# Kernel tuning notes

Measured on AMD Instinct MI355X. Metric: run time of the kernel, lower is better.

The kernel has to match this reference:

```python
import jax, jax.numpy as jnp
import numpy as np

K = 3        # kernel_size
PAD = 1      # padding
STRIDE = 1   # stride


def conv2d(x, w, stride, pad):
    return jax.lax.conv_general_dilated(
        x, w, (stride, stride), [(pad, pad), (pad, pad)],
        dimension_numbers=('NCHW', 'OIHW', 'NCHW'))


def setup_inputs() -> dict:
    key = jax.random.key(0)
    ks = jax.random.split(key, 6)
    B, C, H, W, O = 8, 64, 64, 64, 128
    N = K * K
    x = jax.random.normal(ks[0], (B, C, H, W), jnp.float32)
    # offset (shift) conv: 2N output channels; small weights so sampled
    # positions deviate a few pixels from the regular grid
    shift_w = jax.random.normal(ks[1], (2 * N, C, 3, 3), jnp.float32) * 0.01
    shift_b = jax.random.normal(ks[2], (2 * N,), jnp.float32) * 0.5
    # modulation conv: N output channels
    mod_w = jax.random.normal(ks[3], (N, C, 3, 3), jnp.float32) * 0.01
    mod_b = jax.random.normal(ks[4], (N,), jnp.float32) * 0.1
    # final conv (bias=False), applied with stride=K on the unfolded map
    conv_w = jax.random.normal(ks[5], (O, C, K, K), jnp.float32) / np.sqrt(C * K * K)
    return {'x': x, 'shift_w': shift_w, 'shift_b': shift_b,
            'mod_w': mod_w, 'mod_b': mod_b, 'conv_w': conv_w}


def reference(x, shift_w, shift_b, mod_w, mod_b, conv_w):
    B, C, H, W = x.shape
    k = conv_w.shape[-1]
    N = k * k
    # offsets and modulation from 3x3 convs on the raw input
    offset = conv2d(x, shift_w, STRIDE, 1) + shift_b[None, :, None, None]   # (B,2N,H,W)
    modulation = jax.nn.sigmoid(conv2d(x, mod_w, STRIDE, 1) + mod_b[None, :, None, None])  # (B,N,H,W)

    xp = jnp.pad(x, ((0, 0), (0, 0), (PAD, PAD), (PAD, PAD)))  # zero padding
    Hp, Wp = xp.shape[2], xp.shape[3]

    # p_n: kernel-relative offsets, ij meshgrid, x-block then y-block -> (2N,)
    r = (k - 1) // 2
    pn_x, pn_y = jnp.meshgrid(jnp.arange(-r, r + 1), jnp.arange(-r, r + 1), indexing='ij')
    pn = jnp.concatenate([pn_x.ravel(), pn_y.ravel()]).astype(x.dtype)
    # p_0: base grid starts at 1 (accounts for padding)
    p0x = jnp.broadcast_to(jnp.arange(1, H * STRIDE + 1, STRIDE, dtype=x.dtype)[:, None], (H, W))
    p0y = jnp.broadcast_to(jnp.arange(1, W * STRIDE + 1, STRIDE, dtype=x.dtype)[None, :], (H, W))
    p0 = jnp.concatenate([jnp.broadcast_to(p0x, (N, H, W)),
                          jnp.broadcast_to(p0y, (N, H, W))], 0)  # (2N,H,W)

    pos = offset + pn[None, :, None, None] + p0[None]            # (B,2N,H,W)
    pos = jnp.transpose(pos, (0, 2, 3, 1))                       # (B,H,W,2N)
    px, py = pos[..., :N], pos[..., N:]

    # NOTE: original clamps to output H/W (not padded dims) -- kept faithfully
    fx, fy = jnp.floor(px), jnp.floor(py)
    lt_x = jnp.clip(fx, 0, H - 1).astype(jnp.int32)
    lt_y = jnp.clip(fy, 0, W - 1).astype(jnp.int32)
    rb_x = jnp.clip(fx + 1, 0, H - 1).astype(jnp.int32)
    rb_y = jnp.clip(fy + 1, 0, W - 1).astype(jnp.int32)
    # original casts clamped position to long -> integer bilinear weights
    p_x = jnp.clip(px, 0, H - 1).astype(jnp.int32)
    p_y = jnp.clip(py, 0, W - 1).astype(jnp.int32)

    g_lt = ((1 + (lt_x - p_x)) * (1 + (lt_y - p_y))).astype(x.dtype)
    g_rb = ((1 - (rb_x - p_x)) * (1 - (rb_y - p_y))).astype(x.dtype)
    g_lb = ((1 + (lt_x - p_x)) * (1 + (rb_y - p_y))).astype(x.dtype)  # lb=(lt_x,rb_y)
    g_rt = ((1 - (rb_x - p_x)) * (1 - (lt_y - p_y))).astype(x.dtype)  # rt=(rb_x,lt_y)

    x_flat = xp.reshape(B, C, Hp * Wp)

    def gather(qx, qy):
        idx = (qx * Wp + qy).reshape(B, 1, -1)                     # (B,1,H*W*N)
        v = jnp.take_along_axis(x_flat, jnp.broadcast_to(idx, (B, C, idx.shape[-1])), axis=-1)
        return v.reshape(B, C, H, W, N)

    x_off = (g_lt[:, None] * gather(lt_x, lt_y)
             + g_rb[:, None] * gather(rb_x, rb_y)
             + g_lb[:, None] * gather(lt_x, rb_y)
             + g_rt[:, None] * gather(rb_x, lt_y))                 # (B,C,H,W,N)

    mod = jnp.transpose(modulation, (0, 2, 3, 1))[:, None]        # (B,1,H,W,N)
    x_off = x_off * mod

    # unfold: out[h*k+a, w*k+b] = x_off[h, w, a*k+b]
    x_off = x_off.reshape(B, C, H, W, k, k).transpose(0, 1, 2, 4, 3, 5).reshape(B, C, H * k, W * k)
    return conv2d(x_off, conv_w, k, 0)                            # (B,O,H,W)
```

## Files before the change

kernel.cpp:

```cpp
#include <hip/hip_runtime.h>
#include <hip/hip_fp16.h>
#include <math.h>


typedef _Float16 half8_t __attribute__((ext_vector_type(8)));
typedef float f32x4 __attribute__((ext_vector_type(4)));

__global__ __launch_bounds__(256) void k_pre(const float* __restrict__ x,
                                             const float* __restrict__ cw,
                                             const float* __restrict__ shift_w,
                                             const float* __restrict__ mod_w,
                                             __half* __restrict__ xTh,
                                             __half* __restrict__ xTl,
                                             __half* __restrict__ xCb,
                                             __half* __restrict__ WtF,
                                             __half* __restrict__ WtSFh,
                                             __half* __restrict__ WtSFl) {
    __shared__ float tile[64][65];
    int bid = blockIdx.x;
    int t = threadIdx.x;
    if (bid < 512) {
        int b = bid >> 6, pt = bid & 63;
        int lane = t & 63, cq = t >> 6;
        const float* xb = x + ((size_t)b << 18);
#pragma unroll
        for (int r = 0; r < 16; ++r) {
            int c = cq * 16 + r;
            tile[c][lane] = xb[((size_t)c << 12) + pt * 64 + lane];
        }
        __syncthreads();
        int p = t >> 2, qc = t & 3;
        __align__(16) _Float16 hh[16];
        __align__(16) _Float16 ll[16];
        __align__(16) _Float16 cb[16];
#pragma unroll
        for (int k = 0; k < 16; ++k) {
            float v0 = tile[qc * 16 + k][p];
            float v1 = (p < 63) ? tile[qc * 16 + k][p + 1] : 0.f;
            _Float16 h = (_Float16)v0;
            hh[k] = h;
            ll[k] = (_Float16)(v0 - (float)h);
            cb[k] = (_Float16)(v0 + 2.f * v1);
        }
        size_t off = ((size_t)b << 18) + (size_t)(pt * 64 + p) * 64 + qc * 16;
        ((uint4*)(xTh + off))[0] = ((uint4*)hh)[0];
        ((uint4*)(xTh + off))[1] = ((uint4*)hh)[1];
        ((uint4*)(xTl + off))[0] = ((uint4*)ll)[0];
        ((uint4*)(xTl + off))[1] = ((uint4*)ll)[1];
        ((uint4*)(xCb + off))[0] = ((uint4*)cb)[0];
        ((uint4*)(xCb + off))[1] = ((uint4*)cb)[1];
    } else {
        int u = (bid - 512) * 256 + t;
        if (u < 73728) {
            int e = u & 7, l = (u >> 3) & 63, ks = (u >> 9) & 1;
            int g = (u >> 10) & 3, w = (u >> 12) & 1, n = u >> 13;
            int o = w * 64 + g * 16 + (l & 15);
            int c = ks * 32 + (l >> 4) * 8 + e;
            WtF[u] = __float2half_rn(cw[(o * 64 + c) * 9 + n]);
        } else {
            int q = u - 73728;
            if (q < 18432) {
                int e = q & 7, l = (q >> 3) & 63, nf = (q >> 9) & 1;
                int chf = (q >> 10) & 1, tap = q >> 11;
                int ch = nf * 16 + (l & 15);
                int c = chf * 32 + (l >> 4) * 8 + e;
                float wv = 0.f;
                if (ch < 18) wv = shift_w[(ch * 64 + c) * 9 + tap];
                else if (ch < 27) wv = mod_w[((ch - 18) * 64 + c) * 9 + tap];
                _Float16 h = (_Float16)wv;
                _Float16 lo = (_Float16)(wv - (float)h);
                WtSFh[q] = *(__half*)&h;
                WtSFl[q] = *(__half*)&lo;
            }
        }
    }
}

__device__ __forceinline__ void combine_frag(uint4 rc, bool simple, float mod,
                                             const uint4& g0, const uint4& g1,
                                             const uint4& g2, const uint4& g3,
                                             __half2* a2) {
    if (simple) {
        __half mh = __float2half_rn(mod);
        __half2 mm(mh, mh);
        const __half2* vv = (const __half2*)&g0;
        a2[0] = __hmul2(mm, vv[0]);
        a2[1] = __hmul2(mm, vv[1]);
        a2[2] = __hmul2(mm, vv[2]);
        a2[3] = __hmul2(mm, vv[3]);
    } else {
        a2[0] = __half2(0, 0); a2[1] = __half2(0, 0);
        a2[2] = __half2(0, 0); a2[3] = __half2(0, 0);
        const uint4* grs[4] = {&g0, &g1, &g2, &g3};
#pragma unroll
        for (int jq = 0; jq < 4; ++jq) {
            float wf = (float)((rc.x >> (24 + 2 * jq)) & 3) * mod;
            __half2 wh2 = __half2(__float2half_rn(wf), __float2half_rn(wf));
            const __half2* vv = (const __half2*)grs[jq];
            a2[0] = __hfma2(wh2, vv[0], a2[0]);
            a2[1] = __hfma2(wh2, vv[1], a2[1]);
            a2[2] = __hfma2(wh2, vv[2], a2[2]);
            a2[3] = __hfma2(wh2, vv[3], a2[3]);
        }
    }
}

__global__ __launch_bounds__(512, 2) void k_fused(
    const __half* __restrict__ xTh, const __half* __restrict__ xTl,
    const __half* __restrict__ xCb, const __half* __restrict__ WtF,
    const __half* __restrict__ WtSFh, const __half* __restrict__ WtSFl,
    const float* __restrict__ shift_b, const float* __restrict__ mod_b,
    float* __restrict__ out) {
    __shared__ __align__(16) unsigned char arena[50688];
    __shared__ float Cw[2][4][16][36];
    __shared__ uint4 recA[9][64];

    int t = threadIdx.x;
    int l = t & 63;
    int w = t >> 6;
    int l15 = l & 15, lhi = l >> 4;

    int bid = blockIdx.x;
    int bk = (bid & 7) * 64 + (bid >> 3);
    int b = bk >> 6;
    int row = bk & 63;

    const __half* xbh = xTh + ((size_t)b << 18);
    const __half* xbl = xTl + ((size_t)b << 18);
    const __half* xbc = xCb + ((size_t)b << 18);

#pragma unroll
    for (int rr = 0; rr < 7; ++rr) {
        int d = rr * 512 + t;
        if (d < 3168) {
            int bufl = d >= 1584 ? 1 : 0;
            int dd = d - bufl * 1584;
            int s = dd >> 3, cb8 = dd & 7;
            int r = s / 66, j = s - r * 66;
            int grow = row + r - 1;
            int gcol = j - 1;
            uint4 v = make_uint4(0u, 0u, 0u, 0u);
            if ((unsigned)grow < 64u && (unsigned)gcol < 64u) {
                const __half* src = (bufl ? xbl : xbh) +
                                    ((size_t)((grow << 6) + gcol) << 6) + (cb8 << 3);
                v = *(const uint4*)src;
            }
            int dst = bufl * 25344 + s * 128 + ((cb8 << 4) ^ ((s & 7) << 4));
            *(uint4*)&arena[dst] = v;
        }
    }
    __syncthreads();

    {
        int wp = w >> 1, wh = w & 1;
        f32x4 aP[2], aQ[2], aR[2];
#pragma unroll
        for (int nf = 0; nf < 2; ++nf) {
            aP[nf] = (f32x4){0.f, 0.f, 0.f, 0.f};
            aQ[nf] = (f32x4){0.f, 0.f, 0.f, 0.f};
            aR[nf] = (f32x4){0.f, 0.f, 0.f, 0.f};
        }
#pragma unroll
        for (int tr = 0; tr < 3; ++tr)
#pragma unroll
            for (int tc = 0; tc < 3; ++tc) {
                int tap = tr * 3 + tc;
                int j = wp * 16 + l15 + tc;
                int s = tr * 66 + j;
                int cbyte = (wh << 6) + (lhi << 4);
                int addr = s * 128 + (cbyte ^ ((s & 7) << 4));
                half8_t Ah = *(const half8_t*)&arena[addr];
                half8_t Al = *(const half8_t*)&arena[25344 + addr];
#pragma unroll
                for (int nf = 0; nf < 2; ++nf) {
                    int fo = ((((tap << 1) + wh) << 1) + nf) << 9;
                    half8_t Bh = *(const half8_t*)(WtSFh + fo + (l << 3));
                    half8_t Bl = *(const half8_t*)(WtSFl + fo + (l << 3));
                    aP[nf] = __builtin_amdgcn_mfma_f32_16x16x32_f16(Ah, Bh, aP[nf], 0, 0, 0);
                    aQ[nf] = __builtin_amdgcn_mfma_f32_16x16x32_f16(Ah, Bl, aQ[nf], 0, 0, 0);
                    aR[nf] = __builtin_amdgcn_mfma_f32_16x16x32_f16(Al, Bh, aR[nf], 0, 0, 0);
                }
            }
#pragma unroll
        for (int nf = 0; nf < 2; ++nf)
#pragma unroll
            for (int v4 = 0; v4 < 4; ++v4)
                Cw[wh][wp][(lhi << 2) + v4][nf * 16 + l15] =
                    (aP[nf][v4] + aQ[nf][v4]) + aR[nf][v4];
    }
    __syncthreads();

#pragma unroll
    for (int jj0 = 0; jj0 < 2; ++jj0) {
        int rid = jj0 * 512 + t;
        if (rid < 576) {
            int p = rid & 63;
            int n = rid >> 6;
            int wp = p >> 4, pp = p & 15;
            float sx = Cw[0][wp][pp][n] + Cw[1][wp][pp][n];
            float sy = Cw[0][wp][pp][9 + n] + Cw[1][wp][pp][9 + n];
            float sm = Cw[0][wp][pp][18 + n] + Cw[1][wp][pp][18 + n];

            float px = ((sx + shift_b[n]) + (float)(n / 3 - 1)) + (float)(row + 1);
            float py = ((sy + shift_b[9 + n]) + (float)(n % 3 - 1)) + (float)(p + 1);
            float mod = 1.f / (1.f + expf(-(sm + mod_b[n])));

            float fx = floorf(px), fy = floorf(py);
            int ltx = (int)fminf(fmaxf(fx, 0.f), 63.f);
            int lty = (int)fminf(fmaxf(fy, 0.f), 63.f);
            int rbx = (int)fminf(fmaxf(fx + 1.f, 0.f), 63.f);
            int rby = (int)fminf(fmaxf(fy + 1.f, 0.f), 63.f);
            int pxi = (int)fminf(fmaxf(px, 0.f), 63.f);
            int pyi = (int)fminf(fmaxf(py, 0.f), 63.f);

            int g_lt = (1 + ltx - pxi) * (1 + lty - pyi);
            int g_rb = (1 - rbx + pxi) * (1 - rby + pyi);
            int g_lb = (1 + ltx - pxi) * (1 + rby - pyi);
            int g_rt = (1 - rbx + pxi) * (1 - lty + pyi);

            bool simple = (ltx == pxi) && (lty == pyi) && (rbx == pxi + 1) &&
                          (rby == pyi + 1) && (ltx >= 1) && (lty >= 1);

            int qxa[4] = {ltx, rbx, ltx, rbx};
            int qya[4] = {lty, rby, rby, lty};
            int gga[4] = {g_lt, g_rb, g_lb, g_rt};
            unsigned w0 = 0, w1 = 0;
#pragma unroll
            for (int jq = 0; jq < 4; ++jq) {
                bool valid = (qxa[jq] >= 1) && (qya[jq] >= 1);
                unsigned idx = valid ? (unsigned)((qxa[jq] - 1) * 64 + (qya[jq] - 1)) : 0u;
                unsigned gc = valid ? (unsigned)gga[jq] : 0u;
                if (jq < 2) w0 |= idx << (12 * jq); else w1 |= idx << (12 * (jq - 2));
                w0 |= gc << (24 + 2 * jq);
            }
            if (simple) w1 |= 0x80000000u;
            recA[n][p] = make_uint4(w0, w1, __float_as_uint(mod), 0u);
        }
    }
    __syncthreads();

    int wm = w >> 1, wn = w & 1;
    int mA = t >> 3, cg = t & 7;

    f32x4 acc[4];
#pragma unroll
    for (int g = 0; g < 4; ++g) acc[g] = (f32x4){0.f, 0.f, 0.f, 0.f};

    {
        const uint4* wsrc = (const uint4*)WtF;
        uint4* wdst = (uint4*)&arena[16384];
        wdst[t] = wsrc[t];
        wdst[512 + t] = wsrc[512 + t];

        uint4 rc = recA[0][mA];
        bool smp = (rc.y >> 31) != 0u;
        uint4 g0, g1, g2, g3;
        if (smp) {
            g0 = *(const uint4*)(xbc + ((int)(rc.x & 0xFFF) << 6) + (cg << 3));
        } else {
            g0 = *(const uint4*)(xbh + ((int)(rc.x & 0xFFF) << 6) + (cg << 3));
            g1 = *(const uint4*)(xbh + ((int)((rc.x >> 12) & 0xFFF) << 6) + (cg << 3));
            g2 = *(const uint4*)(xbh + ((int)(rc.y & 0xFFF) << 6) + (cg << 3));
            g3 = *(const uint4*)(xbh + ((int)((rc.y >> 12) & 0xFFF) << 6) + (cg << 3));
        }
        __align__(16) __half2 a2[4];
        combine_frag(rc, smp, __uint_as_float(rc.z), g0, g1, g2, g3, a2);
        *(uint4*)&arena[(mA << 7) | ((cg ^ (mA & 7)) << 4)] = *(uint4*)a2;
    }
    __syncthreads();

    for (int n = 0; n < 9; ++n) {
        int sl = n & 1;

        uint4 wv0, wv1, rcN;
        uint4 gr0, gr1, gr2, gr3;
        bool simpleN = false;
        if (n < 8) {
            const uint4* wsrc = (const uint4*)(WtF + (n + 1) * 8192);
            wv0 = wsrc[t];
            wv1 = wsrc[512 + t];
            rcN = recA[n + 1][mA];
            simpleN = (rcN.y >> 31) != 0u;
            if (simpleN) {
                gr0 = *(const uint4*)(xbc + ((int)(rcN.x & 0xFFF) << 6) + (cg << 3));
            } else {
                gr0 = *(const uint4*)(xbh + ((int)(rcN.x & 0xFFF) << 6) + (cg << 3));
                gr1 = *(const uint4*)(xbh + ((int)((rcN.x >> 12) & 0xFFF) << 6) + (cg << 3));
                gr2 = *(const uint4*)(xbh + ((int)(rcN.y & 0xFFF) << 6) + (cg << 3));
                gr3 = *(const uint4*)(xbh + ((int)((rcN.y >> 12) & 0xFFF) << 6) + (cg << 3));
            }
        }

        {
            const unsigned char* wsl = &arena[16384 + (sl << 14)];
#pragma unroll
            for (int ks = 0; ks < 2; ++ks) {
                int rowa = wm * 16 + l15;
                int gr = (ks * 4 + lhi) ^ (rowa & 7);
                half8_t Af = *(const half8_t*)&arena[(sl << 13) | (rowa << 7) | (gr << 4)];
#pragma unroll
                for (int g = 0; g < 4; ++g) {
                    half8_t Bf = *(const half8_t*)&wsl[((((wn << 2) + g) << 1) + ks) * 1024 +
                                                       (l << 4)];
                    acc[g] = __builtin_amdgcn_mfma_f32_16x16x32_f16(Af, Bf, acc[g], 0, 0, 0);
                }
            }
        }

        if (n < 8) {
            int s2 = sl ^ 1;
            uint4* wdst = (uint4*)&arena[16384 + (s2 << 14)];
            wdst[t] = wv0;
            wdst[512 + t] = wv1;

            __align__(16) __half2 a2[4];
            combine_frag(rcN, simpleN, __uint_as_float(rcN.z), gr0, gr1, gr2, gr3, a2);
            *(uint4*)&arena[(s2 << 13) | (mA << 7) | ((cg ^ (mA & 7)) << 4)] =
                *(uint4*)a2;
            __syncthreads();
        }
    }

    {
        float* ob = out + ((size_t)b << 19);
        int prow = (row << 6) + (wm << 4) + (lhi << 2);
#pragma unroll
        for (int g = 0; g < 4; ++g) {
            int o = (wn << 6) + (g << 4) + l15;
            float* dst = ob + (((size_t)o) << 12) + prow;
            *(float4*)dst = *(float4*)&acc[g];
        }
    }
}

extern "C" void kernel_launch(void* const* d_in, const int* in_sizes, int n_in,
                              void* d_out, int out_size, void* d_ws, size_t ws_size,
                              hipStream_t stream) {
    const float* x = (const float*)d_in[0];
    const float* shift_w = (const float*)d_in[1];
    const float* shift_b = (const float*)d_in[2];
    const float* mod_w = (const float*)d_in[3];
    const float* mod_b = (const float*)d_in[4];
    const float* conv_w = (const float*)d_in[5];
    float* out = (float*)d_out;

    char* ws = (char*)d_ws;
    __half* xTh = (__half*)ws;
    __half* xTl = (__half*)(ws + 4194304);
    __half* xCb = (__half*)(ws + 8388608);
    __half* WtF = (__half*)(ws + 12582912);
    __half* WtSFh = (__half*)(ws + 12730368);
    __half* WtSFl = (__half*)(ws + 12767232);

    k_pre<<<dim3(872), dim3(256), 0, stream>>>(x, conv_w, shift_w, mod_w,
                                               xTh, xTl, xCb, WtF, WtSFh, WtSFl);
    k_fused<<<dim3(512), dim3(512), 0, stream>>>(xTh, xTl, xCb, WtF, WtSFh,
                                                 WtSFl, shift_b, mod_b, out);
}
```

Baseline: 35.56 us.

## Chain split-precision MFMAs into one accumulator and stage output through LDS

The offset/modulation conv now accumulates the hi*hi, hi*lo and lo*hi fp16 MFMA products into a single accumulator per fragment instead of three, which frees registers but serializes the MFMA dependency chain. The __syncthreads in the main loop moves outside the conditional. The epilogue writes the accumulators into a padded LDS tile and then has each thread store contiguous float4 chunks, so global output writes are coalesced. This adds an extra barrier and LDS round trip per block.

```diff
diff --git a/kernel.cpp b/kernel.cpp
--- a/kernel.cpp
+++ b/kernel.cpp
@@ -153,13 +153,9 @@
 
     {
         int wp = w >> 1, wh = w & 1;
-        f32x4 aP[2], aQ[2], aR[2];
-#pragma unroll
-        for (int nf = 0; nf < 2; ++nf) {
-            aP[nf] = (f32x4){0.f, 0.f, 0.f, 0.f};
-            aQ[nf] = (f32x4){0.f, 0.f, 0.f, 0.f};
-            aR[nf] = (f32x4){0.f, 0.f, 0.f, 0.f};
-        }
+        f32x4 accA[2];
+        accA[0] = (f32x4){0.f, 0.f, 0.f, 0.f};
+        accA[1] = (f32x4){0.f, 0.f, 0.f, 0.f};
 #pragma unroll
         for (int tr = 0; tr < 3; ++tr)
 #pragma unroll
@@ -176,17 +172,16 @@
                     int fo = ((((tap << 1) + wh) << 1) + nf) << 9;
                     half8_t Bh = *(const half8_t*)(WtSFh + fo + (l << 3));
                     half8_t Bl = *(const half8_t*)(WtSFl + fo + (l << 3));
-                    aP[nf] = __builtin_amdgcn_mfma_f32_16x16x32_f16(Ah, Bh, aP[nf], 0, 0, 0);
-                    aQ[nf] = __builtin_amdgcn_mfma_f32_16x16x32_f16(Ah, Bl, aQ[nf], 0, 0, 0);
-                    aR[nf] = __builtin_amdgcn_mfma_f32_16x16x32_f16(Al, Bh, aR[nf], 0, 0, 0);
+                    accA[nf] = __builtin_amdgcn_mfma_f32_16x16x32_f16(Ah, Bh, accA[nf], 0, 0, 0);
+                    accA[nf] = __builtin_amdgcn_mfma_f32_16x16x32_f16(Ah, Bl, accA[nf], 0, 0, 0);
+                    accA[nf] = __builtin_amdgcn_mfma_f32_16x16x32_f16(Al, Bh, accA[nf], 0, 0, 0);
                 }
             }
 #pragma unroll
         for (int nf = 0; nf < 2; ++nf)
 #pragma unroll
             for (int v4 = 0; v4 < 4; ++v4)
-                Cw[wh][wp][(lhi << 2) + v4][nf * 16 + l15] =
-                    (aP[nf][v4] + aQ[nf][v4]) + aR[nf][v4];
+                Cw[wh][wp][(lhi << 2) + v4][nf * 16 + l15] = accA[nf][v4];
     }
     __syncthreads();
 
@@ -317,18 +312,33 @@
             combine_frag(rcN, simpleN, __uint_as_float(rcN.z), gr0, gr1, gr2, gr3, a2);
             *(uint4*)&arena[(s2 << 13) | (mA << 7) | ((cg ^ (mA & 7)) << 4)] =
                 *(uint4*)a2;
-            __syncthreads();
-        }
-    }
-
+        }
+        __syncthreads();
+    }
+
+    float* Ep = (float*)arena;
+#pragma unroll
+    for (int g = 0; g < 4; ++g) {
+        int o_loc = (wn << 6) + (g << 4) + l15;
+#pragma unroll
+        for (int v4 = 0; v4 < 4; ++v4)
+            Ep[o_loc * 65 + (wm << 4) + (lhi << 2) + v4] = acc[g][v4];
+    }
+    __syncthreads();
     {
         float* ob = out + ((size_t)b << 19);
-        int prow = (row << 6) + (wm << 4) + (lhi << 2);
-#pragma unroll
-        for (int g = 0; g < 4; ++g) {
-            int o = (wn << 6) + (g << 4) + l15;
-            float* dst = ob + (((size_t)o) << 12) + prow;
-            *(float4*)dst = *(float4*)&acc[g];
+        int prow = row << 6;
+#pragma unroll
+        for (int r = 0; r < 4; ++r) {
+            int o_loc = (r << 5) + (t >> 4);
+            int mseg = t & 15;
+            float4 fa;
+            fa.x = Ep[o_loc * 65 + mseg * 4 + 0];
+            fa.y = Ep[o_loc * 65 + mseg * 4 + 1];
+            fa.z = Ep[o_loc * 65 + mseg * 4 + 2];
+            fa.w = Ep[o_loc * 65 + mseg * 4 + 3];
+            float* dst = ob + (((size_t)o_loc) << 12) + prow + mseg * 4;
+            *(float4*)dst = fa;
         }
     }
 }
```

New measurement: 34.91 us. Within noise of the previous version (-1.8%).
